# Kernel tuning notes

Hardware: AMD Instinct MI355X
Metric: run time of the kernel (lower is better)

Reference implementation:

```python
import jax, jax.numpy as jnp
import numpy as np

N_BIT = 4
GROUP = 128
ALPHA_W = 1.0   # group_size > -1 forces weight alpha to 1.0
ALPHA_A = 0.9   # searched input alpha
TOKENS, D_IN, D_OUT = 2048, 2048, 2048


def _int_grid(n_bit):
    B = n_bit - 1
    v = [0.0] + [float(s * i) for i in range(1, 2 ** B) for s in (1, -1)]
    v = np.sort(np.asarray(v, np.float32)) * (32.0 / 2 ** B)
    return v


def _outlier_grid(n_bit, exp_bit=2, exp_base=5):
    B = n_bit - 1
    mant_bit = B - exp_bit
    vals = []
    for i in range(exp_base, exp_base + 2 ** exp_bit):
        for j in range(2 ** mant_bit):
            if i == exp_base and j == 0:
                continue
            v = 2.0 ** i * (1.0 + 2.0 ** (-mant_bit) * j)
            vals += [v, -v]
    return np.sort(np.asarray(vals, np.float32))


_QG = _int_grid(N_BIT)
MAX_Q = float(_QG.max())              # 28.0 for 4-bit int grid
MERGED_GRID = jnp.asarray(np.concatenate([_QG, _outlier_grid(N_BIT)]))  # [29]


def get_quant(x, alpha, group_size):
    """Faithful jax port of get_quant(): per-group scale, nearest merged-grid
    quantization, roll-based outlier/victim masking, fp16 dequant."""
    org_shape = x.shape
    if group_size == -2:
        t = x.reshape(-1)
        mean, std = t.mean(), t.std(ddof=1)
    else:
        t = x.reshape(-1, group_size) if group_size > 0 else x
        mean = t.mean(axis=1, keepdims=True)
        std = t.std(axis=1, ddof=1, keepdims=True)
    normal_max = jnp.maximum(jnp.abs(mean + 3 * std), jnp.abs(mean - 3 * std))
    scales = normal_max * alpha / MAX_Q
    # nearest grid point over merged quant+outlier grid (the chunk loop in the
    # original is memory-chunking only; math is identical done whole)
    labels = jnp.argmin(jnp.abs((t / scales)[..., None] - MERGED_GRID), axis=-1)
    qf = MERGED_GRID[labels].reshape(-1)
    # victim masking: outliers (|q|>32) steal their paired neighbor's slot
    mask = jnp.abs(qf) > 32.0
    victim_odd = jnp.roll(mask, 1).at[::2].set(False)
    victim_even = jnp.roll(mask & ~victim_odd, -1).at[1::2].set(False)
    qf = jnp.where(victim_odd | victim_even, 0.0, qf)
    if group_size >= -1:
        qf = qf.reshape(t.shape)
    deq = (qf * scales).astype(jnp.float16)
    return deq.reshape(org_shape)


def setup_inputs() -> dict:
    key = jax.random.key(0)
    k1, k2 = jax.random.split(key)
    x = jax.random.normal(k1, (TOKENS, D_IN), dtype=jnp.float32)
    weight = jax.random.normal(k2, (D_OUT, D_IN), dtype=jnp.float32) * 0.02
    return {"x": x, "weight": weight}


def reference(x, weight):
    # runtime path of OliVe_Linear.forward (post-calibration), group_size=128
    w_deq = get_quant(weight, ALPHA_W, GROUP).astype(jnp.float32)
    x_deq = get_quant(x, ALPHA_A, GROUP).astype(jnp.float32)
    return x_deq @ w_deq.T  # [tokens, out_features]
```

## Files before the change

### kernel.cpp

```cpp
#include <hip/hip_runtime.h>
#include <hip/hip_fp16.h>
#include <stdint.h>

#define TOKENS 2048
#define DIM    2048
#define GROUP  128
#define NGK    16

typedef __attribute__((ext_vector_type(4)))  int   i32x4;
typedef __attribute__((ext_vector_type(16))) int   i32x16;
typedef __attribute__((ext_vector_type(4)))  float f32x4;
typedef __attribute__((ext_vector_type(16))) float f32x16;


__device__ __forceinline__ float nearest_q4(float u) {
  float qi = fminf(fmaxf(rintf(u), -7.f), 7.f);
  float a = fabsf(u);
  float m = a <= 14.f ? 12.f : a <= 20.f ? 16.f : a <= 28.f ? 24.f
          : a <= 40.f ? 32.f : a <= 56.f ? 48.f : a <= 80.f ? 64.f : 96.f;
  float qo = copysignf(m, u);
  return (fabsf(u - qo) < fabsf(u - qi)) ? qo : qi;
}

__global__ __launch_bounds__(256) void quant2_kernel(
    const float* __restrict__ x, const float* __restrict__ w,
    int8_t* __restrict__ q8,
    float* __restrict__ ssxT,
    float* __restrict__ sswT) {
  const int wid  = threadIdx.x >> 6;
  const int lane = threadIdx.x & 63;
  const int l    = lane & 31;
  const int g    = blockIdx.x * 8 + wid * 2 + (lane >> 5);
  const int NG1  = TOKENS * DIM / GROUP;

  const float alpha = (g < NG1) ? 0.9f : 1.0f;
  const float* src  = (g < NG1) ? x : w;
  const int grow    = (g < NG1) ? g : g - NG1;
  const size_t sbase = (size_t)grow * GROUP + l * 4;

  const float4 v = *reinterpret_cast<const float4*>(src + sbase);

  float s  = (v.x + v.y) + (v.z + v.w);
  float ss = fmaf(v.x, v.x, fmaf(v.y, v.y, fmaf(v.z, v.z, v.w * v.w)));
#pragma unroll
  for (int off = 16; off > 0; off >>= 1) {
    s  += __shfl_xor(s,  off, 64);
    ss += __shfl_xor(ss, off, 64);
  }
  const float mean = s * (1.0f / 128.0f);
  const float var  = fmaf(-mean, s, ss) * (1.0f / 127.0f);
  const float scale = fmaf(3.0f, sqrtf(var), fabsf(mean)) * (alpha / 28.0f);
  const float rs4 = 0.25f / scale;

  const float u0 = v.x * rs4, u1 = v.y * rs4, u2 = v.z * rs4, u3 = v.w * rs4;
  const float amax = fmaxf(fmaxf(fabsf(u0), fabsf(u1)),
                           fmaxf(fabsf(u2), fabsf(u3)));

  int i0, i1, i2, i3;
  if (__any(amax >= 9.5f)) {
    float q0 = nearest_q4(u0);
    float q1 = nearest_q4(u1);
    float q2 = nearest_q4(u2);
    float q3 = nearest_q4(u3);
    if (fabsf(q0) > 8.0f)      q1 = 0.0f;
    else if (fabsf(q1) > 8.0f) q0 = 0.0f;
    if (fabsf(q2) > 8.0f)      q3 = 0.0f;
    else if (fabsf(q3) > 8.0f) q2 = 0.0f;
    i0 = (int)q0; i1 = (int)q1; i2 = (int)q2; i3 = (int)q3;
  } else {
    i0 = (int)fminf(fmaxf(rintf(u0), -7.f), 7.f);
    i1 = (int)fminf(fmaxf(rintf(u1), -7.f), 7.f);
    i2 = (int)fminf(fmaxf(rintf(u2), -7.f), 7.f);
    i3 = (int)fminf(fmaxf(rintf(u3), -7.f), 7.f);
  }

  const int p = (i0 & 255) | ((i1 & 255) << 8) |
                ((i2 & 255) << 16) | ((i3 & 255) << 24);
  reinterpret_cast<int*>(q8)[(size_t)g * 32 + l] = p;

  if (l == 0) {
    const float ssc = 4.0f * scale;
    if (g < NG1) ssxT[(grow & 15) * 2048 + (grow >> 4)] = ssc;
    else         sswT[(grow & 15) * 2048 + (grow >> 4)] = ssc;
  }
}


__device__ __forceinline__ void gload_lds16(const int8_t* g, char* l) {
  __builtin_amdgcn_global_load_lds(
      (__attribute__((address_space(1))) uint32_t*)g,
      (__attribute__((address_space(3))) uint32_t*)l, 16, 0, 0);
}

__global__ __launch_bounds__(256, 2) void gemm_kernel(
    const int8_t* __restrict__ Aq, const int8_t* __restrict__ Bq,
    const float* __restrict__ ssxT, const float* __restrict__ sswT,
    float* __restrict__ C) {
  __shared__ char lds_raw[2 * 24576 + 12288];
  float* ssx_l = (float*)(lds_raw + 49152);
  float* ssw_l = (float*)(lds_raw + 49152 + 8192);

  const int tid  = threadIdx.x;
  const int lane = tid & 63;
  const int wid  = tid >> 6;
  const int wr   = wid >> 1;
  const int wc   = wid & 1;
  const int r31  = lane & 31;
  const int hi   = lane >> 5;

  const int bid = blockIdx.x;
  const int c   = bid & 7;
  const int idx = bid >> 3;
  const int bm  = ((c & 3) << 2) + (idx >> 4);
  const int bn  = ((c >> 2) << 4) + (idx & 15);

  const int8_t* gA = Aq + (size_t)(bm * 128) * DIM;
  const int8_t* gB = Bq + (size_t)(bn * 64) * DIM;

  auto stage = [&](char* buf, int g) {
#pragma unroll
    for (int i = 0; i < 4; ++i) {
      int P   = (i * 256 + tid) * 16;
      int row = P >> 7;
      int cb  = (P & 127) ^ ((row & 7) << 4);
      gload_lds16(gA + (size_t)row * DIM + g * 128 + cb, buf + P);
    }
#pragma unroll
    for (int i = 0; i < 2; ++i) {
      int P   = (i * 256 + tid) * 16;
      int row = P >> 7;
      int cb  = (P & 127) ^ ((row & 7) << 4);
      gload_lds16(gB + (size_t)row * DIM + g * 128 + cb, buf + 16384 + P);
    }
  };

#pragma unroll
  for (int i = 0; i < 2; ++i) {
    int f = (i * 256 + tid) * 4;
    *reinterpret_cast<f32x4*>(&ssx_l[f]) =
        *reinterpret_cast<const f32x4*>(&ssxT[(f >> 7) * 2048 + bm * 128 + (f & 127)]);
  }
  {
    int f = tid * 4;
    *reinterpret_cast<f32x4*>(&ssw_l[f]) =
        *reinterpret_cast<const f32x4*>(&sswT[(f >> 6) * 2048 + bn * 64 + (f & 63)]);
  }
  __syncthreads();

  f32x16 accf[2] = {};
  const i32x16 zacc = {};

  auto compute = [&](const char* buf, int gk) {
    const char* cA = buf;
    const char* cB = buf + 16384;
    i32x16 acci[2];
#pragma unroll
    for (int ks = 0; ks < 4; ++ks) {
      const int cb = ks * 32 + hi * 16;
      i32x4 af[2], bf;
#pragma unroll
      for (int mt = 0; mt < 2; ++mt) {
        int row = wr * 64 + mt * 32 + r31;
        int pc  = cb ^ ((row & 7) << 4);
        af[mt] = *reinterpret_cast<const i32x4*>(cA + (row << 7) + pc);
      }
      {
        int row = wc * 32 + r31;
        int pc  = cb ^ ((row & 7) << 4);
        bf = *reinterpret_cast<const i32x4*>(cB + (row << 7) + pc);
      }
      __builtin_amdgcn_s_setprio(1);
#pragma unroll
      for (int mt = 0; mt < 2; ++mt)
        acci[mt] = __builtin_amdgcn_mfma_i32_32x32x32_i8(
            af[mt], bf, ks == 0 ? zacc : acci[mt], 0, 0, 0);
      __builtin_amdgcn_s_setprio(0);
    }
    const float sw = ssw_l[gk * 64 + wc * 32 + r31];
#pragma unroll
    for (int mt = 0; mt < 2; ++mt)
#pragma unroll
      for (int q = 0; q < 4; ++q) {
        f32x4 sx = *reinterpret_cast<const f32x4*>(
            &ssx_l[gk * 128 + wr * 64 + mt * 32 + 8 * q + 4 * hi]);
#pragma unroll
        for (int e = 0; e < 4; ++e)
          accf[mt][q * 4 + e] += sx[e] * (sw * (float)acci[mt][q * 4 + e]);
      }
  };

  char* S0 = lds_raw;
  char* S1 = lds_raw + 24576;

  stage(S0, 0);
  for (int j = 0; j < NGK; ++j) {
    if (j + 1 < NGK) {
      stage((j & 1) ? S0 : S1, j + 1);
      asm volatile("s_waitcnt vmcnt(6)" ::: "memory");
    } else {
      asm volatile("s_waitcnt vmcnt(0)" ::: "memory");
    }
    __builtin_amdgcn_s_barrier();
    compute((j & 1) ? S1 : S0, j);
    __builtin_amdgcn_s_barrier();
  }

  const int crow0 = bm * 128 + wr * 64 + 4 * hi;
  const int ccol  = bn * 64 + wc * 32 + r31;
#pragma unroll
  for (int mt = 0; mt < 2; ++mt)
#pragma unroll
    for (int r = 0; r < 16; ++r) {
      int row = crow0 + mt * 32 + (r & 3) + 8 * (r >> 2);
      C[(size_t)row * DIM + ccol] = accf[mt][r];
    }
}


extern "C" void kernel_launch(void* const* d_in, const int* in_sizes, int n_in,
                              void* d_out, int out_size, void* d_ws,
                              size_t ws_size, hipStream_t stream) {
  const float* x = (const float*)d_in[0];
  const float* w = (const float*)d_in[1];
  float* out = (float*)d_out;

  int8_t* qx   = (int8_t*)d_ws;
  int8_t* qw   = qx + (size_t)TOKENS * DIM;
  float*  ssxT = (float*)(qw + (size_t)DIM * DIM);
  float*  sswT = ssxT + NGK * 2048;

  const int ngroups = 2 * TOKENS * DIM / GROUP;
  quant2_kernel<<<ngroups / 8, 256, 0, stream>>>(x, w, qx, ssxT, sswT);

  gemm_kernel<<<512, 256, 0, stream>>>(qx, qw, ssxT, sswT, out);
}
```

Baseline: 33.09 us.

## Halve GEMM M-tile to 64 and switch to 16x16x64 int8 MFMA

The GEMM tile shrinks from 128x64 to 64x64, doubling the grid to 1024 blocks. LDS use drops so four blocks can fit per CU, and each wave now uses 2x2 mfma_i32_16x16x64_i8 tiles instead of 32x32x32. The aim is more parallelism and occupancy to hide latency in this small problem. In exchange, each block reuses less data (more global/L2 traffic per FLOP), and the rescale work per MFMA is relatively higher.

```diff
diff --git a/kernel.cpp b/kernel.cpp
--- a/kernel.cpp
+++ b/kernel.cpp
@@ -8,9 +8,7 @@
 #define NGK    16
 
 typedef __attribute__((ext_vector_type(4)))  int   i32x4;
-typedef __attribute__((ext_vector_type(16))) int   i32x16;
 typedef __attribute__((ext_vector_type(4)))  float f32x4;
-typedef __attribute__((ext_vector_type(16))) float f32x16;
 
 
 __device__ __forceinline__ float nearest_q4(float u) {
@@ -92,34 +90,34 @@
       (__attribute__((address_space(3))) uint32_t*)l, 16, 0, 0);
 }
 
-__global__ __launch_bounds__(256, 2) void gemm_kernel(
+__global__ __launch_bounds__(256, 4) void gemm_kernel(
     const int8_t* __restrict__ Aq, const int8_t* __restrict__ Bq,
     const float* __restrict__ ssxT, const float* __restrict__ sswT,
     float* __restrict__ C) {
-  __shared__ char lds_raw[2 * 24576 + 12288];
-  float* ssx_l = (float*)(lds_raw + 49152);
-  float* ssw_l = (float*)(lds_raw + 49152 + 8192);
+  __shared__ char lds_raw[2 * 16384 + 8192];
+  float* ssx_l = (float*)(lds_raw + 32768);
+  float* ssw_l = (float*)(lds_raw + 32768 + 4096);
 
   const int tid  = threadIdx.x;
   const int lane = tid & 63;
   const int wid  = tid >> 6;
   const int wr   = wid >> 1;
   const int wc   = wid & 1;
-  const int r31  = lane & 31;
-  const int hi   = lane >> 5;
+  const int r15  = lane & 15;
+  const int hi4  = lane >> 4;
 
   const int bid = blockIdx.x;
   const int c   = bid & 7;
   const int idx = bid >> 3;
-  const int bm  = ((c & 3) << 2) + (idx >> 4);
+  const int bm  = ((c & 3) << 3) + (idx >> 4);
   const int bn  = ((c >> 2) << 4) + (idx & 15);
 
-  const int8_t* gA = Aq + (size_t)(bm * 128) * DIM;
+  const int8_t* gA = Aq + (size_t)(bm * 64) * DIM;
   const int8_t* gB = Bq + (size_t)(bn * 64) * DIM;
 
   auto stage = [&](char* buf, int g) {
 #pragma unroll
-    for (int i = 0; i < 4; ++i) {
+    for (int i = 0; i < 2; ++i) {
       int P   = (i * 256 + tid) * 16;
       int row = P >> 7;
       int cb  = (P & 127) ^ ((row & 7) << 4);
@@ -130,15 +128,14 @@
       int P   = (i * 256 + tid) * 16;
       int row = P >> 7;
       int cb  = (P & 127) ^ ((row & 7) << 4);
-      gload_lds16(gB + (size_t)row * DIM + g * 128 + cb, buf + 16384 + P);
+      gload_lds16(gB + (size_t)row * DIM + g * 128 + cb, buf + 8192 + P);
     }
   };
 
-#pragma unroll
-  for (int i = 0; i < 2; ++i) {
-    int f = (i * 256 + tid) * 4;
+  {
+    int f = tid * 4;
     *reinterpret_cast<f32x4*>(&ssx_l[f]) =
-        *reinterpret_cast<const f32x4*>(&ssxT[(f >> 7) * 2048 + bm * 128 + (f & 127)]);
+        *reinterpret_cast<const f32x4*>(&ssxT[(f >> 6) * 2048 + bm * 64 + (f & 63)]);
   }
   {
     int f = tid * 4;
@@ -147,56 +144,62 @@
   }
   __syncthreads();
 
-  f32x16 accf[2] = {};
-  const i32x16 zacc = {};
+  f32x4 accf[2][2] = {};
+  const i32x4 zacc = {};
 
   auto compute = [&](const char* buf, int gk) {
     const char* cA = buf;
-    const char* cB = buf + 16384;
-    i32x16 acci[2];
-#pragma unroll
-    for (int ks = 0; ks < 4; ++ks) {
-      const int cb = ks * 32 + hi * 16;
-      i32x4 af[2], bf;
+    const char* cB = buf + 8192;
+    i32x4 acci[2][2];
+#pragma unroll
+    for (int kh = 0; kh < 2; ++kh) {
+      const int kb = kh * 64 + hi4 * 16;
+      i32x4 af[2], bf[2];
 #pragma unroll
       for (int mt = 0; mt < 2; ++mt) {
-        int row = wr * 64 + mt * 32 + r31;
-        int pc  = cb ^ ((row & 7) << 4);
+        int row = wr * 32 + mt * 16 + r15;
+        int pc  = kb ^ ((row & 7) << 4);
         af[mt] = *reinterpret_cast<const i32x4*>(cA + (row << 7) + pc);
       }
-      {
-        int row = wc * 32 + r31;
-        int pc  = cb ^ ((row & 7) << 4);
-        bf = *reinterpret_cast<const i32x4*>(cB + (row << 7) + pc);
+#pragma unroll
+      for (int nt = 0; nt < 2; ++nt) {
+        int row = wc * 32 + nt * 16 + r15;
+        int pc  = kb ^ ((row & 7) << 4);
+        bf[nt] = *reinterpret_cast<const i32x4*>(cB + (row << 7) + pc);
       }
       __builtin_amdgcn_s_setprio(1);
 #pragma unroll
       for (int mt = 0; mt < 2; ++mt)
-        acci[mt] = __builtin_amdgcn_mfma_i32_32x32x32_i8(
-            af[mt], bf, ks == 0 ? zacc : acci[mt], 0, 0, 0);
+#pragma unroll
+        for (int nt = 0; nt < 2; ++nt)
+          acci[mt][nt] = __builtin_amdgcn_mfma_i32_16x16x64_i8(
+              af[mt], bf[nt], kh == 0 ? zacc : acci[mt][nt], 0, 0, 0);
       __builtin_amdgcn_s_setprio(0);
     }
-    const float sw = ssw_l[gk * 64 + wc * 32 + r31];
-#pragma unroll
-    for (int mt = 0; mt < 2; ++mt)
-#pragma unroll
-      for (int q = 0; q < 4; ++q) {
-        f32x4 sx = *reinterpret_cast<const f32x4*>(
-            &ssx_l[gk * 128 + wr * 64 + mt * 32 + 8 * q + 4 * hi]);
+    float sw[2];
+#pragma unroll
+    for (int nt = 0; nt < 2; ++nt)
+      sw[nt] = ssw_l[gk * 64 + wc * 32 + nt * 16 + r15];
+#pragma unroll
+    for (int mt = 0; mt < 2; ++mt) {
+      f32x4 sx = *reinterpret_cast<const f32x4*>(
+          &ssx_l[gk * 64 + wr * 32 + mt * 16 + 4 * hi4]);
+#pragma unroll
+      for (int nt = 0; nt < 2; ++nt)
 #pragma unroll
         for (int e = 0; e < 4; ++e)
-          accf[mt][q * 4 + e] += sx[e] * (sw * (float)acci[mt][q * 4 + e]);
-      }
+          accf[mt][nt][e] += sx[e] * (sw[nt] * (float)acci[mt][nt][e]);
+    }
   };
 
   char* S0 = lds_raw;
-  char* S1 = lds_raw + 24576;
+  char* S1 = lds_raw + 16384;
 
   stage(S0, 0);
   for (int j = 0; j < NGK; ++j) {
     if (j + 1 < NGK) {
       stage((j & 1) ? S0 : S1, j + 1);
-      asm volatile("s_waitcnt vmcnt(6)" ::: "memory");
+      asm volatile("s_waitcnt vmcnt(4)" ::: "memory");
     } else {
       asm volatile("s_waitcnt vmcnt(0)" ::: "memory");
     }
@@ -205,15 +208,18 @@
     __builtin_amdgcn_s_barrier();
   }
 
-  const int crow0 = bm * 128 + wr * 64 + 4 * hi;
-  const int ccol  = bn * 64 + wc * 32 + r31;
+  const int crow0 = bm * 64 + wr * 32 + 4 * hi4;
+  const int ccol0 = bn * 64 + wc * 32 + r15;
 #pragma unroll
   for (int mt = 0; mt < 2; ++mt)
 #pragma unroll
-    for (int r = 0; r < 16; ++r) {
-      int row = crow0 + mt * 32 + (r & 3) + 8 * (r >> 2);
-      C[(size_t)row * DIM + ccol] = accf[mt][r];
-    }
+    for (int nt = 0; nt < 2; ++nt)
+#pragma unroll
+      for (int r = 0; r < 4; ++r) {
+        int row = crow0 + mt * 16 + r;
+        int col = ccol0 + nt * 16;
+        C[(size_t)row * DIM + col] = accf[mt][nt][r];
+      }
 }
 
 
@@ -232,5 +238,5 @@
   const int ngroups = 2 * TOKENS * DIM / GROUP;
   quant2_kernel<<<ngroups / 8, 256, 0, stream>>>(x, w, qx, ssxT, sswT);
 
-  gemm_kernel<<<512, 256, 0, stream>>>(qx, qw, ssxT, sswT, out);
-}
+  gemm_kernel<<<1024, 256, 0, stream>>>(qx, qw, ssxT, sswT, out);
+}
```

Result: faster. 31.53 us (median of 2 runs) (-4.7%).
